# Kernel tuning notes

Measured on AMD Instinct MI355X. Metric: run time of the kernel, lower is better.

## Reference

```python
import jax, jax.numpy as jnp
import numpy as np
import math

N_EMBD = 768
N_HEAD = 12
B, T = 4, 2048
HEAD_DIM = N_EMBD // N_HEAD


def new_gelu(x):
    # GPT-2 tanh approximation of GELU (NewGELUActivation)
    c = math.sqrt(2.0 / math.pi)
    return 0.5 * x * (1.0 + jnp.tanh(c * (x + 0.044715 * jnp.power(x, 3.0))))


def layer_norm(x, g, b, eps=1e-5):
    mu = jnp.mean(x, axis=-1, keepdims=True)
    var = jnp.mean(jnp.square(x - mu), axis=-1, keepdims=True)
    return (x - mu) * jax.lax.rsqrt(var + eps) * g + b


def setup_inputs() -> dict:
    key = jax.random.key(0)
    ks = jax.random.split(key, 12)
    s = 0.02
    return {
        "x": jax.random.normal(ks[0], (B, T, N_EMBD), dtype=jnp.float32),
        "ln1_g": jnp.ones((N_EMBD,), jnp.float32),
        "ln1_b": jnp.zeros((N_EMBD,), jnp.float32),
        "W_attn": jax.random.normal(ks[1], (N_EMBD, 3 * N_EMBD), jnp.float32) * s,
        "b_attn": jnp.zeros((3 * N_EMBD,), jnp.float32),
        "W_proj": jax.random.normal(ks[2], (N_EMBD, N_EMBD), jnp.float32) * s,
        "b_proj": jnp.zeros((N_EMBD,), jnp.float32),
        "ln2_g": jnp.ones((N_EMBD,), jnp.float32),
        "ln2_b": jnp.zeros((N_EMBD,), jnp.float32),
        "W_fc": jax.random.normal(ks[3], (N_EMBD, 4 * N_EMBD), jnp.float32) * s,
        "b_fc": jnp.zeros((4 * N_EMBD,), jnp.float32),
        "W_fc2": jax.random.normal(ks[4], (4 * N_EMBD, N_EMBD), jnp.float32) * s,
        "b_fc2": jnp.zeros((N_EMBD,), jnp.float32),
    }


def block_forward(x, ln1_g, ln1_b, W_attn, b_attn, W_proj, b_proj,
                  ln2_g, ln2_b, W_fc, b_fc, W_fc2, b_fc2):
    # ---- attention sublayer (pre-LN) ----
    h = layer_norm(x, ln1_g, ln1_b)
    qkv = h @ W_attn + b_attn                      # [B,T,3C]
    q, k, v = jnp.split(qkv, 3, axis=-1)
    q = q.reshape(B, T, N_HEAD, HEAD_DIM).transpose(0, 2, 1, 3)  # [B,H,T,D]
    k = k.reshape(B, T, N_HEAD, HEAD_DIM).transpose(0, 2, 1, 3)
    v = v.reshape(B, T, N_HEAD, HEAD_DIM).transpose(0, 2, 1, 3)
    scores = jnp.einsum('bhqd,bhkd->bhqk', q, k) / math.sqrt(HEAD_DIM)
    causal = jnp.tril(jnp.ones((T, T), dtype=bool))
    scores = jnp.where(causal[None, None, :, :], scores, -jnp.inf)
    attn = jax.nn.softmax(scores, axis=-1)
    y = jnp.einsum('bhqk,bhkd->bhqd', attn, v)      # [B,H,T,D]
    y = y.transpose(0, 2, 1, 3).reshape(B, T, N_EMBD)
    y = y @ W_proj + b_proj
    x = x + y
    # ---- MLP sublayer ----
    h = layer_norm(x, ln2_g, ln2_b)
    h = new_gelu(h @ W_fc + b_fc)
    h = h @ W_fc2 + b_fc2
    return x + h


def reference(x, ln1_g, ln1_b, W_attn, b_attn, W_proj, b_proj,
              ln2_g, ln2_b, W_fc, b_fc, W_fc2, b_fc2):
    return block_forward(x, ln1_g, ln1_b, W_attn, b_attn, W_proj, b_proj,
                         ln2_g, ln2_b, W_fc, b_fc, W_fc2, b_fc2)
```

## Files before the change

### kernel.cpp

```cpp
#include <hip/hip_runtime.h>
#include <hip/hip_bf16.h>

typedef __attribute__((ext_vector_type(8))) short short8;
typedef __attribute__((ext_vector_type(4))) float f32x4;
typedef __attribute__((ext_vector_type(8))) unsigned short u16x8;
typedef __attribute__((ext_vector_type(4))) unsigned short u16x4;

#define MFMA16(A, B, C) __builtin_amdgcn_mfma_f32_16x16x32_bf16(A, B, C, 0, 0, 0)

static __device__ __forceinline__ unsigned short f2bf(float f) {
    unsigned int u = __builtin_bit_cast(unsigned int, f);
    u += 0x7FFF + ((u >> 16) & 1);
    return (unsigned short)(u >> 16);
}

static __device__ __forceinline__ unsigned int cvt_pk_bf16(float a, float b) {
    unsigned int r;
    asm("v_cvt_pk_bf16_f32 %0, %1, %2" : "=v"(r) : "v"(a), "v"(b));
    return r;
}

static __device__ __forceinline__ float gelu_f(float v) {
    const float k1 = 2.3022077646f;
    const float k2 = 0.1029432207f;
    float t = __builtin_amdgcn_exp2f(-(k1 * v + k2 * v * v * v));
    return v * __builtin_amdgcn_rcpf(1.0f + t);
}

typedef const __attribute__((address_space(1))) unsigned int* gas_t;
typedef __attribute__((address_space(3))) unsigned int* las_t;
static __device__ __forceinline__ void gl_lds16(const void* g, void* l) {
    __builtin_amdgcn_global_load_lds((gas_t)g, (las_t)l, 16, 0, 0);
}

__global__ void wtrans(const float* __restrict__ W, unsigned short* __restrict__ Wt,
                       int K, int N) {
    __shared__ float tl[32][33];
    const int n0 = blockIdx.x * 32, k0 = blockIdx.y * 32;
    const int tx = threadIdx.x, ty = threadIdx.y;
#pragma unroll
    for (int i = 0; i < 4; i++)
        tl[ty + 8 * i][tx] = W[(long)(k0 + ty + 8 * i) * N + n0 + tx];
    __syncthreads();
#pragma unroll
    for (int i = 0; i < 4; i++)
        Wt[(long)(n0 + ty + 8 * i) * K + k0 + tx] = f2bf(tl[tx][ty + 8 * i]);
}

__global__ __launch_bounds__(256)
void ln_fwd(const float* __restrict__ x, const float* __restrict__ gw,
            const float* __restrict__ bw, unsigned short* __restrict__ out) {
    const int row = blockIdx.x * 4 + (threadIdx.x >> 6);
    const int ln = threadIdx.x & 63;
    const float4* xr = (const float4*)(x + (long)row * 768);
    float4 v[3];
    float s = 0.f;
#pragma unroll
    for (int j = 0; j < 3; j++) {
        v[j] = xr[ln + 64 * j];
        s += v[j].x + v[j].y + v[j].z + v[j].w;
    }
#pragma unroll
    for (int off = 32; off >= 1; off >>= 1) s += __shfl_xor(s, off);
    const float mean = s * (1.0f / 768.0f);
    float sq = 0.f;
#pragma unroll
    for (int j = 0; j < 3; j++) {
        float a = v[j].x - mean, b = v[j].y - mean, c = v[j].z - mean, d = v[j].w - mean;
        sq += a * a + b * b + c * c + d * d;
    }
#pragma unroll
    for (int off = 32; off >= 1; off >>= 1) sq += __shfl_xor(sq, off);
    const float rstd = rsqrtf(sq * (1.0f / 768.0f) + 1e-5f);
#pragma unroll
    for (int j = 0; j < 3; j++) {
        const int c = ln + 64 * j;
        float4 gg = ((const float4*)gw)[c];
        float4 bb = ((const float4*)bw)[c];
        u16x4 o;
        o[0] = f2bf((v[j].x - mean) * rstd * gg.x + bb.x);
        o[1] = f2bf((v[j].y - mean) * rstd * gg.y + bb.y);
        o[2] = f2bf((v[j].z - mean) * rstd * gg.z + bb.z);
        o[3] = f2bf((v[j].w - mean) * rstd * gg.w + bb.w);
        *(u16x4*)(out + (long)row * 768 + c * 4) = o;
    }
}

template <int MODE, int BN>
__global__ __launch_bounds__(256)
void gemm_bt(const unsigned short* __restrict__ A, const unsigned short* __restrict__ Bt,
             const float* __restrict__ bias, const float* __restrict__ resid,
             void* __restrict__ Out, unsigned short* __restrict__ vT,
             int M, int N, int K) {
    constexpr int NW = BN / 32;
    constexpr int BUF = (128 + BN) * 32;
    constexpr int STN = (BN == 128) ? 132 : 68;
    constexpr int BYTES_MAIN = 2 * BUF * 2;
    constexpr int BYTES_ST = 64 * STN * 4;
    constexpr int BYTES = BYTES_MAIN > BYTES_ST ? BYTES_MAIN : BYTES_ST;
    __shared__ char smem[BYTES];
    unsigned short* ubase = (unsigned short*)smem;
    float* st = (float*)smem;

    const int tid = threadIdx.x;
    const int wv = tid >> 6, ln = tid & 63;
    const int wr = wv >> 1, wc = wv & 1;
    const int g = ln >> 4, r = ln & 15;
    const int sr = ln >> 2, sc = ln & 3;
    const int ssw = sc ^ ((sr >> 1) & 3);
    const long mbase = (long)blockIdx.x * 128;
    const long nbase = (long)blockIdx.y * BN;

    f32x4 acc[4][NW];
    const f32x4 zero = {0.f, 0.f, 0.f, 0.f};
#pragma unroll
    for (int m = 0; m < 4; m++)
#pragma unroll
        for (int n = 0; n < NW; n++) acc[m][n] = zero;

    const int nt = K >> 5;
#pragma unroll
    for (int p = 0; p < 2; p++)
        gl_lds16(A + (mbase + p * 64 + wv * 16 + sr) * (long)K + ssw * 8,
                 ubase + (p * 64 + wv * 16) * 32);
#pragma unroll
    for (int p = 0; p < BN / 64; p++)
        gl_lds16(Bt + (nbase + p * 64 + wv * 16 + sr) * (long)K + ssw * 8,
                 ubase + 128 * 32 + (p * 64 + wv * 16) * 32);
    __syncthreads();

    const int cx = (r >> 1) & 3;
    for (int t = 0; t < nt; t++) {
        const unsigned short* cbuf = ubase + (t & 1) * BUF;
        if (t + 1 < nt) {
            unsigned short* nbuf = ubase + ((t + 1) & 1) * BUF;
            const long k0 = (long)(t + 1) << 5;
#pragma unroll
            for (int p = 0; p < 2; p++)
                gl_lds16(A + (mbase + p * 64 + wv * 16 + sr) * (long)K + k0 + ssw * 8,
                         nbuf + (p * 64 + wv * 16) * 32);
#pragma unroll
            for (int p = 0; p < BN / 64; p++)
                gl_lds16(Bt + (nbase + p * 64 + wv * 16 + sr) * (long)K + k0 + ssw * 8,
                         nbuf + 128 * 32 + (p * 64 + wv * 16) * 32);
        }
        short8 af[4], bfr[NW];
#pragma unroll
        for (int m = 0; m < 4; m++)
            af[m] = *(const short8*)(cbuf + (wr * 64 + m * 16 + r) * 32 + ((g ^ cx) * 8));
#pragma unroll
        for (int n = 0; n < NW; n++)
            bfr[n] = *(const short8*)(cbuf + 128 * 32 + (wc * (BN / 2) + n * 16 + r) * 32 + ((g ^ cx) * 8));
#pragma unroll
        for (int m = 0; m < 4; m++)
#pragma unroll
            for (int n = 0; n < NW; n++) acc[m][n] = MFMA16(af[m], bfr[n], acc[m][n]);
        __syncthreads();
    }

    const int tr = tid >> 2, seg = tid & 3;
#pragma unroll 1
    for (int half = 0; half < 2; half++) {
        __syncthreads();
        if (wr == half) {
#pragma unroll
            for (int m = 0; m < 4; m++)
#pragma unroll
                for (int n = 0; n < NW; n++)
#pragma unroll
                    for (int i = 0; i < 4; i++)
                        st[(m * 16 + g * 4 + i) * STN + wc * (BN / 2) + n * 16 + r] = acc[m][n][i];
        }
        __syncthreads();
        const long row = mbase + half * 64 + tr;
        if constexpr (MODE == 1) {
            if (nbase >= 1536) {
                const int tc = tid & 7;
                const int d0 = tid >> 3;
                const long bb = mbase >> 11;
                const int tg0 = (int)(mbase & 2047) + half * 64 + tc * 8;
#pragma unroll
                for (int it = 0; it < 4; it++) {
                    const int dl = it * 32 + d0;
                    const int h = (int)((nbase - 1536) >> 6) + (dl >> 6);
                    const int dd = dl & 63;
                    const float bc = bias[nbase + dl];
                    u16x8 o;
#pragma unroll
                    for (int j = 0; j < 8; j++)
                        o[j] = f2bf(st[(tc * 8 + j) * STN + dl] + bc);
                    *(u16x8*)(vT + ((bb * 12 + h) * 64 + dd) * 2048 + tg0) = o;
                }
            } else {
                const float qs = (nbase < 768) ? 0.18033688011112042f : 1.0f;
                const long cb = nbase + seg * 32;
                unsigned short* op = (unsigned short*)Out + row * N + cb;
#pragma unroll
                for (int u2 = 0; u2 < 4; u2++) {
                    float4 a = *(const float4*)(st + tr * STN + seg * 32 + u2 * 8);
                    float4 b = *(const float4*)(st + tr * STN + seg * 32 + u2 * 8 + 4);
                    float4 ba = ((const float4*)bias)[(cb >> 2) + u2 * 2];
                    float4 bb2 = ((const float4*)bias)[(cb >> 2) + u2 * 2 + 1];
                    a.x = (a.x + ba.x) * qs; a.y = (a.y + ba.y) * qs;
                    a.z = (a.z + ba.z) * qs; a.w = (a.w + ba.w) * qs;
                    b.x = (b.x + bb2.x) * qs; b.y = (b.y + bb2.y) * qs;
                    b.z = (b.z + bb2.z) * qs; b.w = (b.w + bb2.w) * qs;
                    uint4 w;
                    w.x = cvt_pk_bf16(a.x, a.y);
                    w.y = cvt_pk_bf16(a.z, a.w);
                    w.z = cvt_pk_bf16(b.x, b.y);
                    w.w = cvt_pk_bf16(b.z, b.w);
                    *(uint4*)(op + u2 * 8) = w;
                }
            }
        } else if constexpr (MODE == 3) {
            const long cb = nbase + seg * 32;
            unsigned short* op = (unsigned short*)Out + row * N + cb;
#pragma unroll
            for (int u2 = 0; u2 < 4; u2++) {
                float4 a = *(const float4*)(st + tr * STN + seg * 32 + u2 * 8);
                float4 b = *(const float4*)(st + tr * STN + seg * 32 + u2 * 8 + 4);
                float4 ba = ((const float4*)bias)[(cb >> 2) + u2 * 2];
                float4 bb2 = ((const float4*)bias)[(cb >> 2) + u2 * 2 + 1];
                a.x = gelu_f(a.x + ba.x); a.y = gelu_f(a.y + ba.y);
                a.z = gelu_f(a.z + ba.z); a.w = gelu_f(a.w + ba.w);
                b.x = gelu_f(b.x + bb2.x); b.y = gelu_f(b.y + bb2.y);
                b.z = gelu_f(b.z + bb2.z); b.w = gelu_f(b.w + bb2.w);
                uint4 w;
                w.x = cvt_pk_bf16(a.x, a.y);
                w.y = cvt_pk_bf16(a.z, a.w);
                w.z = cvt_pk_bf16(b.x, b.y);
                w.w = cvt_pk_bf16(b.z, b.w);
                *(uint4*)(op + u2 * 8) = w;
            }
        } else {
            const long cb = nbase + seg * 16;
            float* op = (float*)Out + row * N + cb;
            const float* rp = resid + row * N + cb;
#pragma unroll
            for (int u = 0; u < 4; u++) {
                float4 a = *(const float4*)(st + tr * STN + seg * 16 + u * 4);
                float4 ba = ((const float4*)bias)[(cb >> 2) + u];
                float4 rr = ((const float4*)rp)[u];
                a.x += ba.x + rr.x; a.y += ba.y + rr.y;
                a.z += ba.z + rr.z; a.w += ba.w + rr.w;
                ((float4*)op)[u] = a;
            }
        }
    }
}

__global__ __launch_bounds__(256)
void attn_fwd(const unsigned short* __restrict__ qkv, const unsigned short* __restrict__ vT,
              unsigned short* __restrict__ y) {
    const int pair = blockIdx.x;
    const int bh = blockIdx.y;
    const int b = bh / 12, h = bh % 12;
    __shared__ unsigned short Kl[2 * 64 * 64], Vl[2 * 64 * 64], Pl[64 * 72];
    const int tid = threadIdx.x;
    const int wv = tid >> 6, ln = tid & 63;
    const int g = ln >> 4, r = ln & 15;
    const int lr = ln >> 3, l8 = ln & 7;
    const int sw = l8 ^ lr;
    const int rx = r & 7;
    const f32x4 zero = {0.f, 0.f, 0.f, 0.f};

#pragma unroll 1
    for (int qi = 0; qi < 2; qi++) {
        const int qt = qi ? (31 - pair) : pair;
        const int q0 = qt * 64;
        const int q = wv * 16 + r;
        const long qoff = ((long)(b * 2048 + q0 + q)) * 2304 + h * 64;
        short8 bq0 = *(const short8*)(qkv + qoff + g * 8);
        short8 bq1 = *(const short8*)(qkv + qoff + 32 + g * 8);

        float mrow = -1e30f, lrow = 0.0f;
        f32x4 oacc[4];
#pragma unroll
        for (int f = 0; f < 4; f++) oacc[f] = zero;

#pragma unroll
        for (int p = 0; p < 2; p++) {
            const int row = wv * 8 + p * 32 + lr;
            gl_lds16(qkv + ((long)(b * 2048 + row)) * 2304 + 768 + h * 64 + sw * 8,
                     (char*)Kl + (wv * 8 + p * 32) * 128);
            gl_lds16(vT + ((long)(bh * 64 + row)) * 2048 + sw * 8,
                     (char*)Vl + (wv * 8 + p * 32) * 128);
        }
        __syncthreads();

        for (int kt = 0; kt <= qt; ++kt) {
            const unsigned short* Kb = Kl + (kt & 1) * 4096;
            const unsigned short* Vb = Vl + (kt & 1) * 4096;
            if (kt < qt) {
                char* Kn = (char*)Kl + ((kt + 1) & 1) * 8192;
                char* Vn = (char*)Vl + ((kt + 1) & 1) * 8192;
#pragma unroll
                for (int p = 0; p < 2; p++) {
                    const int row = wv * 8 + p * 32 + lr;
                    gl_lds16(qkv + ((long)(b * 2048 + (kt + 1) * 64 + row)) * 2304 + 768 + h * 64 + sw * 8,
                             Kn + (wv * 8 + p * 32) * 128);
                    gl_lds16(vT + ((long)(bh * 64 + row)) * 2048 + (kt + 1) * 64 + sw * 8,
                             Vn + (wv * 8 + p * 32) * 128);
                }
            }

            f32x4 s[4];
#pragma unroll
            for (int kf = 0; kf < 4; kf++) {
                short8 a0 = *(const short8*)(Kb + (kf * 16 + r) * 64 + (g ^ rx) * 8);
                short8 a1 = *(const short8*)(Kb + (kf * 16 + r) * 64 + ((g + 4) ^ rx) * 8);
                s[kf] = MFMA16(a0, bq0, zero);
                s[kf] = MFMA16(a1, bq1, s[kf]);
            }
            if (kt == qt) {
#pragma unroll
                for (int kf = 0; kf < 4; kf++)
#pragma unroll
                    for (int i = 0; i < 4; i++)
                        if (kf * 16 + g * 4 + i > q) s[kf][i] = -1e30f;
            }
            float tmax = -1e30f;
#pragma unroll
            for (int kf = 0; kf < 4; kf++)
#pragma unroll
                for (int i = 0; i < 4; i++) tmax = fmaxf(tmax, s[kf][i]);
            tmax = fmaxf(tmax, __shfl_xor(tmax, 16));
            tmax = fmaxf(tmax, __shfl_xor(tmax, 32));
            if (__any(tmax > mrow + 6.0f)) {
                const float mnew = fmaxf(mrow, tmax);
                const float rs = __builtin_amdgcn_exp2f(mrow - mnew);
                lrow *= rs;
#pragma unroll
                for (int f = 0; f < 4; f++) oacc[f] *= rs;
                mrow = mnew;
            }
            float pv[4][4];
            float psum = 0.f;
#pragma unroll
            for (int kf = 0; kf < 4; kf++)
#pragma unroll
                for (int i = 0; i < 4; i++) {
                    pv[kf][i] = __builtin_amdgcn_exp2f(s[kf][i] - mrow);
                    psum += pv[kf][i];
                }
            psum += __shfl_xor(psum, 16);
            psum += __shfl_xor(psum, 32);
            lrow += psum;

#pragma unroll
            for (int kf = 0; kf < 4; kf++) {
                uint2 w;
                w.x = cvt_pk_bf16(pv[kf][0], pv[kf][1]);
                w.y = cvt_pk_bf16(pv[kf][2], pv[kf][3]);
                *(uint2*)(Pl + q * 72 + kf * 16 + g * 4) = w;
            }
            short8 pb0 = *(const short8*)(Pl + q * 72 + g * 8);
            short8 pb1 = *(const short8*)(Pl + q * 72 + 32 + g * 8);
#pragma unroll
            for (int f = 0; f < 4; f++) {
                short8 va0 = *(const short8*)(Vb + (f * 16 + r) * 64 + (g ^ rx) * 8);
                short8 va1 = *(const short8*)(Vb + (f * 16 + r) * 64 + ((g + 4) ^ rx) * 8);
                oacc[f] = MFMA16(va0, pb0, oacc[f]);
                oacc[f] = MFMA16(va1, pb1, oacc[f]);
            }
            __syncthreads();
        }

        const float inv = 1.0f / lrow;
#pragma unroll
        for (int f = 0; f < 4; f++) {
            uint2 w;
            w.x = cvt_pk_bf16(oacc[f][0] * inv, oacc[f][1] * inv);
            w.y = cvt_pk_bf16(oacc[f][2] * inv, oacc[f][3] * inv);
            *(uint2*)(Pl + q * 72 + f * 16 + g * 4) = w;
        }
        __syncthreads();
#pragma unroll
        for (int p = 0; p < 2; p++) {
            int idx = p * 256 + tid;
            int row = idx >> 3, cc = (idx & 7) * 8;
            *(u16x8*)(y + ((long)(b * 2048 + q0 + row)) * 768 + h * 64 + cc) =
                *(const u16x8*)(Pl + row * 72 + cc);
        }
        __syncthreads();
    }
}

extern "C" void kernel_launch(void* const* d_in, const int* in_sizes, int n_in,
                              void* d_out, int out_size, void* d_ws, size_t ws_size,
                              hipStream_t stream) {
    const float* x      = (const float*)d_in[0];
    const float* ln1_g  = (const float*)d_in[1];
    const float* ln1_b  = (const float*)d_in[2];
    const float* W_attn = (const float*)d_in[3];
    const float* b_attn = (const float*)d_in[4];
    const float* W_proj = (const float*)d_in[5];
    const float* b_proj = (const float*)d_in[6];
    const float* ln2_g  = (const float*)d_in[7];
    const float* ln2_b  = (const float*)d_in[8];
    const float* W_fc   = (const float*)d_in[9];
    const float* b_fc   = (const float*)d_in[10];
    const float* W_fc2  = (const float*)d_in[11];
    const float* b_fc2  = (const float*)d_in[12];

    char* ws = (char*)d_ws;
    size_t off = 0;
    auto alloc = [&](size_t bytes) -> char* {
        char* p = ws + off;
        off += (bytes + 255) & ~(size_t)255;
        return p;
    };
    unsigned short* WtA  = (unsigned short*)alloc((size_t)2304 * 768 * 2);
    unsigned short* WtP  = (unsigned short*)alloc((size_t)768 * 768 * 2);
    unsigned short* WtF  = (unsigned short*)alloc((size_t)3072 * 768 * 2);
    unsigned short* WtF2 = (unsigned short*)alloc((size_t)768 * 3072 * 2);
    unsigned short* bigA = (unsigned short*)alloc((size_t)8192 * 3072 * 2);
    float*          x1   = (float*)alloc((size_t)8192 * 768 * 4);
    unsigned short* bufD = (unsigned short*)alloc((size_t)8192 * 768 * 2);
    unsigned short* vT   = (unsigned short*)alloc((size_t)48 * 64 * 2048 * 2);

    wtrans<<<dim3(72, 24), dim3(32, 8), 0, stream>>>(W_attn, WtA, 768, 2304);
    wtrans<<<dim3(24, 24), dim3(32, 8), 0, stream>>>(W_proj, WtP, 768, 768);
    wtrans<<<dim3(96, 24), dim3(32, 8), 0, stream>>>(W_fc, WtF, 768, 3072);
    wtrans<<<dim3(24, 96), dim3(32, 8), 0, stream>>>(W_fc2, WtF2, 3072, 768);
    ln_fwd<<<2048, 256, 0, stream>>>(x, ln1_g, ln1_b, bufD);
    gemm_bt<1, 128><<<dim3(64, 18), 256, 0, stream>>>(bufD, WtA, b_attn, nullptr, bigA, vT, 8192, 2304, 768);
    attn_fwd<<<dim3(16, 48), 256, 0, stream>>>(bigA, vT, bufD);
    gemm_bt<2, 64><<<dim3(64, 12), 256, 0, stream>>>(bufD, WtP, b_proj, x, x1, nullptr, 8192, 768, 768);
    ln_fwd<<<2048, 256, 0, stream>>>(x1, ln2_g, ln2_b, bufD);
    gemm_bt<3, 128><<<dim3(64, 24), 256, 0, stream>>>(bufD, WtF, b_fc, nullptr, bigA, nullptr, 8192, 3072, 768);
    gemm_bt<4, 64><<<dim3(64, 12), 256, 0, stream>>>(bigA, WtF2, b_fc2, x1, (float*)d_out, nullptr, 8192, 768, 3072);
}
```

Before: 286.3 us.

## Triple-buffer GEMM LDS pipeline with vmcnt waits and single barrier per k-step

Replaces the double-buffered global-to-LDS load loop in gemm_bt with a 3-stage ring buffer that prefetches two k-tiles ahead. Each iteration waits with an explicit s_waitcnt vmcnt that lets the newest stage stay in flight, then issues one raw barrier, instead of a full __syncthreads after the MFMAs. The aim is to hide more global-load latency and drop one barrier per iteration. In exchange the kernel uses 1.5x the LDS, which may lower occupancy, and correctness now depends on the hand-counted vmcnt values.

Result: slower. 299.1 us (+4.5%).

```diff
diff --git a/kernel.cpp b/kernel.cpp
--- a/kernel.cpp
+++ b/kernel.cpp
@@ -31,6 +31,11 @@
 typedef __attribute__((address_space(3))) unsigned int* las_t;
 static __device__ __forceinline__ void gl_lds16(const void* g, void* l) {
     __builtin_amdgcn_global_load_lds((gas_t)g, (las_t)l, 16, 0, 0);
+}
+
+template <int N>
+static __device__ __forceinline__ void wait_vmcnt() {
+    asm volatile("s_waitcnt vmcnt(%0)" :: "n"(N) : "memory");
 }
 
 __global__ void wtrans(const float* __restrict__ W, unsigned short* __restrict__ Wt,
@@ -94,8 +99,9 @@
              int M, int N, int K) {
     constexpr int NW = BN / 32;
     constexpr int BUF = (128 + BN) * 32;
+    constexpr int LPS = 2 + BN / 64;
     constexpr int STN = (BN == 128) ? 132 : 68;
-    constexpr int BYTES_MAIN = 2 * BUF * 2;
+    constexpr int BYTES_MAIN = 3 * BUF * 2;
     constexpr int BYTES_ST = 64 * STN * 4;
     constexpr int BYTES = BYTES_MAIN > BYTES_ST ? BYTES_MAIN : BYTES_ST;
     __shared__ char smem[BYTES];
@@ -118,32 +124,31 @@
 #pragma unroll
         for (int n = 0; n < NW; n++) acc[m][n] = zero;
 
+    auto stage = [&](int tt) {
+        unsigned short* nbuf = ubase + (tt % 3) * BUF;
+        const long k0 = (long)tt << 5;
+#pragma unroll
+        for (int p = 0; p < 2; p++)
+            gl_lds16(A + (mbase + p * 64 + wv * 16 + sr) * (long)K + k0 + ssw * 8,
+                     nbuf + (p * 64 + wv * 16) * 32);
+#pragma unroll
+        for (int p = 0; p < BN / 64; p++)
+            gl_lds16(Bt + (nbase + p * 64 + wv * 16 + sr) * (long)K + k0 + ssw * 8,
+                     nbuf + 128 * 32 + (p * 64 + wv * 16) * 32);
+    };
+
     const int nt = K >> 5;
-#pragma unroll
-    for (int p = 0; p < 2; p++)
-        gl_lds16(A + (mbase + p * 64 + wv * 16 + sr) * (long)K + ssw * 8,
-                 ubase + (p * 64 + wv * 16) * 32);
-#pragma unroll
-    for (int p = 0; p < BN / 64; p++)
-        gl_lds16(Bt + (nbase + p * 64 + wv * 16 + sr) * (long)K + ssw * 8,
-                 ubase + 128 * 32 + (p * 64 + wv * 16) * 32);
-    __syncthreads();
+    stage(0);
+    stage(1);
 
     const int cx = (r >> 1) & 3;
     for (int t = 0; t < nt; t++) {
-        const unsigned short* cbuf = ubase + (t & 1) * BUF;
-        if (t + 1 < nt) {
-            unsigned short* nbuf = ubase + ((t + 1) & 1) * BUF;
-            const long k0 = (long)(t + 1) << 5;
-#pragma unroll
-            for (int p = 0; p < 2; p++)
-                gl_lds16(A + (mbase + p * 64 + wv * 16 + sr) * (long)K + k0 + ssw * 8,
-                         nbuf + (p * 64 + wv * 16) * 32);
-#pragma unroll
-            for (int p = 0; p < BN / 64; p++)
-                gl_lds16(Bt + (nbase + p * 64 + wv * 16 + sr) * (long)K + k0 + ssw * 8,
-                         nbuf + 128 * 32 + (p * 64 + wv * 16) * 32);
-        }
+        if (t + 1 < nt) wait_vmcnt<LPS>();
+        else            wait_vmcnt<0>();
+        __builtin_amdgcn_s_barrier();
+        __builtin_amdgcn_sched_barrier(0);
+        if (t + 2 < nt) stage(t + 2);
+        const unsigned short* cbuf = ubase + (t % 3) * BUF;
         short8 af[4], bfr[NW];
 #pragma unroll
         for (int m = 0; m < 4; m++)
@@ -155,7 +160,6 @@
         for (int m = 0; m < 4; m++)
 #pragma unroll
             for (int n = 0; n < NW; n++) acc[m][n] = MFMA16(af[m], bfr[n], acc[m][n]);
-        __syncthreads();
     }
 
     const int tr = tid >> 2, seg = tid & 3;
```

## Share K/V tile loads across both query tiles in attention block

Applied to the files above, without the earlier changes.

Restructures the attention kernel so that the two query tiles assigned to a block are processed within a single pass over key/value tiles, instead of two sequential passes. Each loaded K/V tile is used for both query tiles while the lower tile is still active, removing the repeated K/V loads and barriers of the first pass. Both sets of softmax state and output accumulators are kept live at once, which raises register pressure and may lower occupancy.

Measured after the change: 282.5 us. About the same (-1.3%).

```diff
diff --git a/kernel.cpp b/kernel.cpp
--- a/kernel.cpp
+++ b/kernel.cpp
@@ -256,6 +256,7 @@
     const int pair = blockIdx.x;
     const int bh = blockIdx.y;
     const int b = bh / 12, h = bh % 12;
+    const int qtA = pair, qtB = 31 - pair;
     __shared__ unsigned short Kl[2 * 64 * 64], Vl[2 * 64 * 64], Pl[64 * 72];
     const int tid = threadIdx.x;
     const int wv = tid >> 6, ln = tid & 63;
@@ -264,110 +265,118 @@
     const int sw = l8 ^ lr;
     const int rx = r & 7;
     const f32x4 zero = {0.f, 0.f, 0.f, 0.f};
+    const int q = wv * 16 + r;
+
+    const long qoffA = ((long)(b * 2048 + qtA * 64 + q)) * 2304 + h * 64;
+    const long qoffB = ((long)(b * 2048 + qtB * 64 + q)) * 2304 + h * 64;
+    short8 bqA0 = *(const short8*)(qkv + qoffA + g * 8);
+    short8 bqA1 = *(const short8*)(qkv + qoffA + 32 + g * 8);
+    short8 bqB0 = *(const short8*)(qkv + qoffB + g * 8);
+    short8 bqB1 = *(const short8*)(qkv + qoffB + 32 + g * 8);
+
+    float mA = -1e30f, lA = 0.0f, mB = -1e30f, lB = 0.0f;
+    f32x4 oA[4], oB[4];
+#pragma unroll
+    for (int f = 0; f < 4; f++) { oA[f] = zero; oB[f] = zero; }
+
+    auto process = [&](const short8& b0, const short8& b1, float& mrow, float& lrow,
+                       f32x4* oacc, bool diag, const unsigned short* Kb,
+                       const unsigned short* Vb) {
+        f32x4 s[4];
+#pragma unroll
+        for (int kf = 0; kf < 4; kf++) {
+            short8 a0 = *(const short8*)(Kb + (kf * 16 + r) * 64 + (g ^ rx) * 8);
+            short8 a1 = *(const short8*)(Kb + (kf * 16 + r) * 64 + ((g + 4) ^ rx) * 8);
+            s[kf] = MFMA16(a0, b0, zero);
+            s[kf] = MFMA16(a1, b1, s[kf]);
+        }
+        if (diag) {
+#pragma unroll
+            for (int kf = 0; kf < 4; kf++)
+#pragma unroll
+                for (int i = 0; i < 4; i++)
+                    if (kf * 16 + g * 4 + i > q) s[kf][i] = -1e30f;
+        }
+        float tmax = -1e30f;
+#pragma unroll
+        for (int kf = 0; kf < 4; kf++)
+#pragma unroll
+            for (int i = 0; i < 4; i++) tmax = fmaxf(tmax, s[kf][i]);
+        tmax = fmaxf(tmax, __shfl_xor(tmax, 16));
+        tmax = fmaxf(tmax, __shfl_xor(tmax, 32));
+        if (__any(tmax > mrow + 6.0f)) {
+            const float mnew = fmaxf(mrow, tmax);
+            const float rs = __builtin_amdgcn_exp2f(mrow - mnew);
+            lrow *= rs;
+#pragma unroll
+            for (int f = 0; f < 4; f++) oacc[f] *= rs;
+            mrow = mnew;
+        }
+        float pv[4][4];
+        float psum = 0.f;
+#pragma unroll
+        for (int kf = 0; kf < 4; kf++)
+#pragma unroll
+            for (int i = 0; i < 4; i++) {
+                pv[kf][i] = __builtin_amdgcn_exp2f(s[kf][i] - mrow);
+                psum += pv[kf][i];
+            }
+        psum += __shfl_xor(psum, 16);
+        psum += __shfl_xor(psum, 32);
+        lrow += psum;
+#pragma unroll
+        for (int kf = 0; kf < 4; kf++) {
+            uint2 w;
+            w.x = cvt_pk_bf16(pv[kf][0], pv[kf][1]);
+            w.y = cvt_pk_bf16(pv[kf][2], pv[kf][3]);
+            *(uint2*)(Pl + q * 72 + kf * 16 + g * 4) = w;
+        }
+        short8 pb0 = *(const short8*)(Pl + q * 72 + g * 8);
+        short8 pb1 = *(const short8*)(Pl + q * 72 + 32 + g * 8);
+#pragma unroll
+        for (int f = 0; f < 4; f++) {
+            short8 va0 = *(const short8*)(Vb + (f * 16 + r) * 64 + (g ^ rx) * 8);
+            short8 va1 = *(const short8*)(Vb + (f * 16 + r) * 64 + ((g + 4) ^ rx) * 8);
+            oacc[f] = MFMA16(va0, pb0, oacc[f]);
+            oacc[f] = MFMA16(va1, pb1, oacc[f]);
+        }
+    };
+
+#pragma unroll
+    for (int p = 0; p < 2; p++) {
+        const int row = wv * 8 + p * 32 + lr;
+        gl_lds16(qkv + ((long)(b * 2048 + row)) * 2304 + 768 + h * 64 + sw * 8,
+                 (char*)Kl + (wv * 8 + p * 32) * 128);
+        gl_lds16(vT + ((long)(bh * 64 + row)) * 2048 + sw * 8,
+                 (char*)Vl + (wv * 8 + p * 32) * 128);
+    }
+    __syncthreads();
+
+    for (int kt = 0; kt <= qtB; ++kt) {
+        const unsigned short* Kb = Kl + (kt & 1) * 4096;
+        const unsigned short* Vb = Vl + (kt & 1) * 4096;
+        if (kt < qtB) {
+            char* Kn = (char*)Kl + ((kt + 1) & 1) * 8192;
+            char* Vn = (char*)Vl + ((kt + 1) & 1) * 8192;
+#pragma unroll
+            for (int p = 0; p < 2; p++) {
+                const int row = wv * 8 + p * 32 + lr;
+                gl_lds16(qkv + ((long)(b * 2048 + (kt + 1) * 64 + row)) * 2304 + 768 + h * 64 + sw * 8,
+                         Kn + (wv * 8 + p * 32) * 128);
+                gl_lds16(vT + ((long)(bh * 64 + row)) * 2048 + (kt + 1) * 64 + sw * 8,
+                         Vn + (wv * 8 + p * 32) * 128);
+            }
+        }
+        if (kt <= qtA) process(bqA0, bqA1, mA, lA, oA, kt == qtA, Kb, Vb);
+        process(bqB0, bqB1, mB, lB, oB, kt == qtB, Kb, Vb);
+        __syncthreads();
+    }
 
 #pragma unroll 1
-    for (int qi = 0; qi < 2; qi++) {
-        const int qt = qi ? (31 - pair) : pair;
-        const int q0 = qt * 64;
-        const int q = wv * 16 + r;
-        const long qoff = ((long)(b * 2048 + q0 + q)) * 2304 + h * 64;
-        short8 bq0 = *(const short8*)(qkv + qoff + g * 8);
-        short8 bq1 = *(const short8*)(qkv + qoff + 32 + g * 8);
-
-        float mrow = -1e30f, lrow = 0.0f;
-        f32x4 oacc[4];
-#pragma unroll
-        for (int f = 0; f < 4; f++) oacc[f] = zero;
-
-#pragma unroll
-        for (int p = 0; p < 2; p++) {
-            const int row = wv * 8 + p * 32 + lr;
-            gl_lds16(qkv + ((long)(b * 2048 + row)) * 2304 + 768 + h * 64 + sw * 8,
-                     (char*)Kl + (wv * 8 + p * 32) * 128);
-            gl_lds16(vT + ((long)(bh * 64 + row)) * 2048 + sw * 8,
-                     (char*)Vl + (wv * 8 + p * 32) * 128);
-        }
-        __syncthreads();
-
-        for (int kt = 0; kt <= qt; ++kt) {
-            const unsigned short* Kb = Kl + (kt & 1) * 4096;
-            const unsigned short* Vb = Vl + (kt & 1) * 4096;
-            if (kt < qt) {
-                char* Kn = (char*)Kl + ((kt + 1) & 1) * 8192;
-                char* Vn = (char*)Vl + ((kt + 1) & 1) * 8192;
-#pragma unroll
-                for (int p = 0; p < 2; p++) {
-                    const int row = wv * 8 + p * 32 + lr;
-                    gl_lds16(qkv + ((long)(b * 2048 + (kt + 1) * 64 + row)) * 2304 + 768 + h * 64 + sw * 8,
-                             Kn + (wv * 8 + p * 32) * 128);
-                    gl_lds16(vT + ((long)(bh * 64 + row)) * 2048 + (kt + 1) * 64 + sw * 8,
-                             Vn + (wv * 8 + p * 32) * 128);
-                }
-            }
-
-            f32x4 s[4];
-#pragma unroll
-            for (int kf = 0; kf < 4; kf++) {
-                short8 a0 = *(const short8*)(Kb + (kf * 16 + r) * 64 + (g ^ rx) * 8);
-                short8 a1 = *(const short8*)(Kb + (kf * 16 + r) * 64 + ((g + 4) ^ rx) * 8);
-                s[kf] = MFMA16(a0, bq0, zero);
-                s[kf] = MFMA16(a1, bq1, s[kf]);
-            }
-            if (kt == qt) {
-#pragma unroll
-                for (int kf = 0; kf < 4; kf++)
-#pragma unroll
-                    for (int i = 0; i < 4; i++)
-                        if (kf * 16 + g * 4 + i > q) s[kf][i] = -1e30f;
-            }
-            float tmax = -1e30f;
-#pragma unroll
-            for (int kf = 0; kf < 4; kf++)
-#pragma unroll
-                for (int i = 0; i < 4; i++) tmax = fmaxf(tmax, s[kf][i]);
-            tmax = fmaxf(tmax, __shfl_xor(tmax, 16));
-            tmax = fmaxf(tmax, __shfl_xor(tmax, 32));
-            if (__any(tmax > mrow + 6.0f)) {
-                const float mnew = fmaxf(mrow, tmax);
-                const float rs = __builtin_amdgcn_exp2f(mrow - mnew);
-                lrow *= rs;
-#pragma unroll
-                for (int f = 0; f < 4; f++) oacc[f] *= rs;
-                mrow = mnew;
-            }
-            float pv[4][4];
-            float psum = 0.f;
-#pragma unroll
-            for (int kf = 0; kf < 4; kf++)
-#pragma unroll
-                for (int i = 0; i < 4; i++) {
-                    pv[kf][i] = __builtin_amdgcn_exp2f(s[kf][i] - mrow);
-                    psum += pv[kf][i];
-                }
-            psum += __shfl_xor(psum, 16);
-            psum += __shfl_xor(psum, 32);
-            lrow += psum;
-
-#pragma unroll
-            for (int kf = 0; kf < 4; kf++) {
-                uint2 w;
-                w.x = cvt_pk_bf16(pv[kf][0], pv[kf][1]);
-                w.y = cvt_pk_bf16(pv[kf][2], pv[kf][3]);
-                *(uint2*)(Pl + q * 72 + kf * 16 + g * 4) = w;
-            }
-            short8 pb0 = *(const short8*)(Pl + q * 72 + g * 8);
-            short8 pb1 = *(const short8*)(Pl + q * 72 + 32 + g * 8);
-#pragma unroll
-            for (int f = 0; f < 4; f++) {
-                short8 va0 = *(const short8*)(Vb + (f * 16 + r) * 64 + (g ^ rx) * 8);
-                short8 va1 = *(const short8*)(Vb + (f * 16 + r) * 64 + ((g + 4) ^ rx) * 8);
-                oacc[f] = MFMA16(va0, pb0, oacc[f]);
-                oacc[f] = MFMA16(va1, pb1, oacc[f]);
-            }
-            __syncthreads();
-        }
-
-        const float inv = 1.0f / lrow;
+    for (int e = 0; e < 2; e++) {
+        const float inv = 1.0f / (e ? lB : lA);
+        const f32x4* oacc = e ? oB : oA;
+        const int q0 = (e ? qtB : qtA) * 64;
 #pragma unroll
         for (int f = 0; f < 4; f++) {
             uint2 w;
```
